# Performance work log

Hardware: AMD Instinct MI355X
Metric: run time of the kernel (lower is better)

## Reference

```python
import jax, jax.numpy as jnp
import numpy as np

N_NODES = 50000
N_EDGES = 800000
D_IN = 128
D_GAT = 128
D_LIN = 512
D_OUT = 4
N_CONVS = 3


def setup_inputs() -> dict:
    key = jax.random.key(0)
    ks = jax.random.split(key, 16)
    s = 1.0 / np.sqrt(D_GAT)
    inp = {
        "x": jax.random.normal(ks[0], (N_NODES, D_IN), dtype=jnp.float32),
        "edge_index": jax.random.randint(ks[1], (2, N_EDGES), 0, N_NODES, dtype=jnp.int64),
        # 3 GATConv layers (input_dim == hidden_gat_dim so params stack)
        "conv_W": jax.random.normal(ks[2], (N_CONVS, D_GAT, D_GAT), dtype=jnp.float32) * s,
        "conv_a_src": jax.random.normal(ks[3], (N_CONVS, D_GAT), dtype=jnp.float32) * s,
        "conv_a_dst": jax.random.normal(ks[4], (N_CONVS, D_GAT), dtype=jnp.float32) * s,
        "conv_b": jnp.zeros((N_CONVS, D_GAT), dtype=jnp.float32),
        # MLP head: 128->512, 512->512, 512->512, 512->4
        "lin_W0": jax.random.normal(ks[5], (D_GAT, D_LIN), dtype=jnp.float32) / np.sqrt(D_GAT),
        "lin_b0": jnp.zeros((D_LIN,), dtype=jnp.float32),
        "lin_W1": jax.random.normal(ks[6], (D_LIN, D_LIN), dtype=jnp.float32) / np.sqrt(D_LIN),
        "lin_b1": jnp.zeros((D_LIN,), dtype=jnp.float32),
        "lin_W2": jax.random.normal(ks[7], (D_LIN, D_LIN), dtype=jnp.float32) / np.sqrt(D_LIN),
        "lin_b2": jnp.zeros((D_LIN,), dtype=jnp.float32),
        "lin_Wout": jax.random.normal(ks[8], (D_LIN, D_OUT), dtype=jnp.float32) / np.sqrt(D_LIN),
        "lin_bout": jnp.zeros((D_OUT,), dtype=jnp.float32),
    }
    return inp


def _gat_layer(x, src, dst, W, a_src, a_dst, b, n):
    """PyG-style single-head GATConv with self loops already in (src, dst)."""
    h = x @ W                                    # [N, F]
    e = (h @ a_src)[src] + (h @ a_dst)[dst]      # per-edge raw score [E]
    e = jax.nn.leaky_relu(e, 0.2)
    # segment softmax over destination node neighborhoods
    m = jax.ops.segment_max(e, dst, num_segments=n)
    ex = jnp.exp(e - m[dst])
    denom = jax.ops.segment_sum(ex, dst, num_segments=n)
    alpha = ex / denom[dst]                      # [E]
    out = jax.ops.segment_sum(alpha[:, None] * h[src], dst, num_segments=n)
    return out + b


def reference(x, edge_index, conv_W, conv_a_src, conv_a_dst, conv_b,
              lin_W0, lin_b0, lin_W1, lin_b1, lin_W2, lin_b2, lin_Wout, lin_bout):
    n = x.shape[0]
    loops = jnp.arange(n, dtype=edge_index.dtype)
    src = jnp.concatenate([edge_index[0], loops])  # add self loops (PyG default)
    dst = jnp.concatenate([edge_index[1], loops])
    for i in range(N_CONVS):
        x = _gat_layer(x, src, dst, conv_W[i], conv_a_src[i], conv_a_dst[i], conv_b[i], n)
        x = jax.nn.leaky_relu(x, 0.2)
    for W, b in ((lin_W0, lin_b0), (lin_W1, lin_b1), (lin_W2, lin_b2)):
        x = jax.nn.relu(x @ W + b)  # F.relu(x, 0.2): 0.2 is truthy inplace flag -> plain relu
    return x @ lin_Wout + lin_bout
```

## Files before the change

kernel.cpp:

```cpp
#include <hip/hip_runtime.h>
#include <hip/hip_bf16.h>

#define NN 50000
#define NE 800000
#define NET (NE + NN)
#define SCAN_NB ((NN + 255) / 256)

static inline int imin(int a, int b) { return a < b ? a : b; }

typedef _Float16 half8 __attribute__((ext_vector_type(8)));
typedef _Float16 half2v __attribute__((ext_vector_type(2)));
typedef float f32x4 __attribute__((ext_vector_type(4)));

__global__ void k_count(const int* __restrict__ edst, int* __restrict__ counts) {
    int e = blockIdx.x * blockDim.x + threadIdx.x;
    if (e >= NET) return;
    int d = (e < NE) ? edst[e] : (e - NE);
    atomicAdd(&counts[d], 1);
}

__global__ __launch_bounds__(256) void k_scan1(const int* __restrict__ counts,
                                               int* __restrict__ part) {
    __shared__ int s[256];
    int t = threadIdx.x, i = blockIdx.x * 256 + t;
    s[t] = (i < NN) ? counts[i] : 0;
    __syncthreads();
    for (int off = 128; off > 0; off >>= 1) {
        if (t < off) s[t] += s[t + off];
        __syncthreads();
    }
    if (t == 0) part[blockIdx.x] = s[0];
}

__global__ __launch_bounds__(256) void k_scan2(int* __restrict__ part, int* __restrict__ offs) {
    __shared__ int s[256];
    int t = threadIdx.x;
    int v = (t < SCAN_NB) ? part[t] : 0;
    s[t] = v;
    __syncthreads();
    for (int off = 1; off < 256; off <<= 1) {
        int a = (t >= off) ? s[t - off] : 0;
        __syncthreads();
        s[t] += a;
        __syncthreads();
    }
    if (t < SCAN_NB) part[t] = s[t] - v;
    if (t == 255) offs[NN] = s[255];
}

__global__ __launch_bounds__(256) void k_scan3(const int* __restrict__ counts,
                                               const int* __restrict__ part,
                                               int* __restrict__ offs, int* __restrict__ cursor) {
    __shared__ int s[256];
    int t = threadIdx.x, i = blockIdx.x * 256 + t;
    int v = (i < NN) ? counts[i] : 0;
    s[t] = v;
    __syncthreads();
    for (int off = 1; off < 256; off <<= 1) {
        int a = (t >= off) ? s[t - off] : 0;
        __syncthreads();
        s[t] += a;
        __syncthreads();
    }
    if (i < NN) {
        int e = part[blockIdx.x] + s[t] - v;
        offs[i] = e;
        cursor[i] = e;
    }
}

__global__ void k_scatter(const int* __restrict__ esrc, const int* __restrict__ edst,
                          int* __restrict__ cursor, int* __restrict__ csr_src) {
    int e = blockIdx.x * blockDim.x + threadIdx.x;
    if (e >= NET) return;
    int s, d;
    if (e < NE) { s = esrc[e]; d = edst[e]; } else { s = e - NE; d = s; }
    int pos = atomicAdd(&cursor[d], 1);
    csr_src[pos] = s;
}

__global__ void k_split(const float* __restrict__ in, _Float16* __restrict__ hi,
                        _Float16* __restrict__ lo, int n) {
    int i = blockIdx.x * blockDim.x + threadIdx.x;
    int st = gridDim.x * blockDim.x;
    for (; i < n; i += st) {
        float v = in[i];
        _Float16 h = (_Float16)v;
        hi[i] = h;
        lo[i] = (_Float16)(v - (float)h);
    }
}

__global__ __launch_bounds__(256) void k_prepw(const float* __restrict__ W,
                                               _Float16* __restrict__ Th,
                                               _Float16* __restrict__ Tl, int K, int N) {
    __shared__ float tile[32][33];
    int tx = threadIdx.x & 31, ty = threadIdx.x >> 5;
    int n0 = blockIdx.x * 32, k0 = blockIdx.y * 32;
    #pragma unroll
    for (int r = ty; r < 32; r += 8)
        tile[r][tx] = W[(size_t)(k0 + r) * N + n0 + tx];
    __syncthreads();
    #pragma unroll
    for (int r = ty; r < 32; r += 8) {
        int n = n0 + r, k = k0 + tx;
        float v = tile[tx][r];
        _Float16 h = (_Float16)v;
        Th[(size_t)n * K + k] = h;
        Tl[(size_t)n * K + k] = (_Float16)(v - (float)h);
    }
}

__global__ void k_aggregate(const _Float16* __restrict__ h, const float* __restrict__ s_src,
                            const float* __restrict__ s_dst, const int* __restrict__ offs,
                            const int* __restrict__ csr_src, const float* __restrict__ bias,
                            _Float16* __restrict__ xh, _Float16* __restrict__ xl) {
    int node = blockIdx.x * 4 + (threadIdx.x >> 6);
    int lane = threadIdx.x & 63;
    if (node >= NN) return;
    int p = offs[node], pe = offs[node + 1];
    float sd = s_dst[node];
    float den = 0.f, acc0 = 0.f, acc1 = 0.f;
    for (; p + 4 <= pe; p += 4) {
        int s0 = csr_src[p + 0], s1 = csr_src[p + 1];
        int s2 = csr_src[p + 2], s3 = csr_src[p + 3];
        float e0 = s_src[s0] + sd, e1 = s_src[s1] + sd;
        float e2 = s_src[s2] + sd, e3 = s_src[s3] + sd;
        half2v a0 = *((const half2v*)(h + (size_t)s0 * 128) + lane);
        half2v a1 = *((const half2v*)(h + (size_t)s1 * 128) + lane);
        half2v a2 = *((const half2v*)(h + (size_t)s2 * 128) + lane);
        half2v a3 = *((const half2v*)(h + (size_t)s3 * 128) + lane);
        e0 = (e0 > 0.f) ? e0 : 0.2f * e0;  float w0 = __expf(e0);
        e1 = (e1 > 0.f) ? e1 : 0.2f * e1;  float w1 = __expf(e1);
        e2 = (e2 > 0.f) ? e2 : 0.2f * e2;  float w2 = __expf(e2);
        e3 = (e3 > 0.f) ? e3 : 0.2f * e3;  float w3 = __expf(e3);
        den += (w0 + w1) + (w2 + w3);
        acc0 += w0 * (float)a0[0] + w1 * (float)a1[0] + w2 * (float)a2[0] + w3 * (float)a3[0];
        acc1 += w0 * (float)a0[1] + w1 * (float)a1[1] + w2 * (float)a2[1] + w3 * (float)a3[1];
    }
    for (; p < pe; ++p) {
        int src = csr_src[p];
        float e = s_src[src] + sd;
        e = (e > 0.f) ? e : 0.2f * e;
        float wgt = __expf(e);
        den += wgt;
        half2v av = *((const half2v*)(h + (size_t)src * 128) + lane);
        acc0 += wgt * (float)av[0];
        acc1 += wgt * (float)av[1];
    }
    float inv = 1.f / den;
    float2 bv = *((const float2*)bias + lane);
    float v0 = acc0 * inv + bv.x;
    float v1 = acc1 * inv + bv.y;
    v0 = (v0 > 0.f) ? v0 : 0.2f * v0;
    v1 = (v1 > 0.f) ? v1 : 0.2f * v1;
    _Float16 h0 = (_Float16)v0, h1 = (_Float16)v1;
    size_t base = (size_t)node * 128 + 2 * lane;
    *(half2v*)(xh + base) = (half2v){h0, h1};
    *(half2v*)(xl + base) = (half2v){(_Float16)(v0 - (float)h0), (_Float16)(v1 - (float)h1)};
}

__device__ __forceinline__ void gload_lds16(const void* g, void* l) {
    __builtin_amdgcn_global_load_lds(
        (const __attribute__((address_space(1))) void*)g,
        (__attribute__((address_space(3))) void*)l, 16, 0, 0);
}

__device__ __forceinline__ void phase_stagger(int bid) {
    int ph = (int)(((unsigned)bid * 2654435761u) >> 29);
    for (int i = 0; i < ph; ++i) __builtin_amdgcn_s_sleep(8);
}

__global__ __launch_bounds__(512) void k_mgemm(
    const _Float16* __restrict__ Ahi, const _Float16* __restrict__ Alo,
    const _Float16* __restrict__ Bhi, const _Float16* __restrict__ Blo,
    const float* __restrict__ bias, float* __restrict__ Cf,
    _Float16* __restrict__ Chi, _Float16* __restrict__ Clo,
    int M, int N, int K, int relu, int split, int nx, int ntiles)
{
    __shared__ _Float16 sm[4][2][128][32];

    int bid = blockIdx.x;
    int per = (ntiles + 7) >> 3;
    int g = (bid & 7) * per + (bid >> 3);
    if (g >= ntiles) return;
    int col0 = (g % nx) * 128;
    int row0 = (g / nx) * 128;

    phase_stagger(bid);

    int t = threadIdx.x;
    int w = t >> 6, lane = t & 63;
    int wm = (w & 3) * 32, wn = (w >> 2) * 64;
    int fr = lane & 15;
    int fq = lane >> 4, fq8 = fq * 8;

    int srow = t >> 2;
    int scol = (t & 3) << 3;
    int lrow = w << 4;

    f32x4 acc[2][4];
    #pragma unroll
    for (int i = 0; i < 2; i++)
        #pragma unroll
        for (int j = 0; j < 4; j++) acc[i][j] = (f32x4){0.f, 0.f, 0.f, 0.f};

    for (int k0 = 0; k0 < K; k0 += 64) {
        if (k0) __syncthreads();
        {
            int ga = row0 + srow; if (ga > M - 1) ga = M - 1;
            int gb = col0 + srow;
            #pragma unroll
            for (int kk = 0; kk < 2; ++kk) {
                int kc = k0 + kk * 32 + scol;
                gload_lds16(Ahi + (size_t)ga * K + kc, &sm[0][kk][lrow][0]);
                gload_lds16(Alo + (size_t)ga * K + kc, &sm[1][kk][lrow][0]);
                gload_lds16(Bhi + (size_t)gb * K + kc, &sm[2][kk][lrow][0]);
                gload_lds16(Blo + (size_t)gb * K + kc, &sm[3][kk][lrow][0]);
            }
        }
        __syncthreads();

        #pragma unroll
        for (int kk = 0; kk < 2; ++kk) {
            half8 bh[4], bl[4];
            #pragma unroll
            for (int ni = 0; ni < 4; ++ni) {
                bh[ni] = *(half8*)&sm[2][kk][wn + ni * 16 + fr][fq8];
                bl[ni] = *(half8*)&sm[3][kk][wn + ni * 16 + fr][fq8];
            }
            #pragma unroll
            for (int mi = 0; mi < 2; ++mi) {
                half8 ah = *(half8*)&sm[0][kk][wm + mi * 16 + fr][fq8];
                half8 al = *(half8*)&sm[1][kk][wm + mi * 16 + fr][fq8];
                #pragma unroll
                for (int ni = 0; ni < 4; ++ni) {
                    acc[mi][ni] = __builtin_amdgcn_mfma_f32_16x16x32_f16(ah, bh[ni], acc[mi][ni], 0, 0, 0);
                    acc[mi][ni] = __builtin_amdgcn_mfma_f32_16x16x32_f16(ah, bl[ni], acc[mi][ni], 0, 0, 0);
                    acc[mi][ni] = __builtin_amdgcn_mfma_f32_16x16x32_f16(al, bh[ni], acc[mi][ni], 0, 0, 0);
                }
            }
        }
    }

    float bv[4];
    #pragma unroll
    for (int ni = 0; ni < 4; ++ni)
        bv[ni] = bias ? bias[col0 + wn + ni * 16 + fr] : 0.f;

    if (split) {
        _Float16* sc = &sm[0][0][0][0];
        #pragma unroll
        for (int pass = 0; pass < 2; ++pass) {
            __syncthreads();
            #pragma unroll
            for (int mi = 0; mi < 2; ++mi) {
                #pragma unroll
                for (int ni = 0; ni < 4; ++ni) {
                    #pragma unroll
                    for (int r = 0; r < 4; ++r) {
                        int row = wm + mi * 16 + fq * 4 + r;
                        int col = wn + ni * 16 + fr;
                        float v = acc[mi][ni][r] + bv[ni];
                        if (relu) v = (v > 0.f) ? v : 0.f;
                        _Float16 hh = (_Float16)v;
                        sc[row * 128 + col] = pass ? (_Float16)(v - (float)hh) : hh;
                    }
                }
            }
            __syncthreads();
            _Float16* dst = pass ? Clo : Chi;
            #pragma unroll
            for (int pp = 0; pp < 4; ++pp) {
                int idx = t + pp * 512;
                int row = idx >> 4, seg = idx & 15;
                int gr = row0 + row;
                if (gr < M)
                    *(half8*)(dst + (size_t)gr * N + col0 + seg * 8) =
                        *(half8*)&sc[row * 128 + seg * 8];
            }
        }
    } else {
        #pragma unroll
        for (int ni = 0; ni < 4; ++ni) {
            #pragma unroll
            for (int mi = 0; mi < 2; ++mi) {
                #pragma unroll
                for (int r = 0; r < 4; ++r) {
                    int gr = row0 + wm + mi * 16 + fq * 4 + r;
                    if (gr >= M) continue;
                    float v = acc[mi][ni][r] + bv[ni];
                    if (relu) v = (v > 0.f) ? v : 0.f;
                    Cf[(size_t)gr * N + col0 + wn + ni * 16 + fr] = v;
                }
            }
        }
    }
}

__global__ __launch_bounds__(512) void k_mgemm_gat(
    const _Float16* __restrict__ Ahi, const _Float16* __restrict__ Alo,
    const _Float16* __restrict__ Bhi, const _Float16* __restrict__ Blo,
    const float* __restrict__ a_src, const float* __restrict__ a_dst,
    _Float16* __restrict__ hbuf, float* __restrict__ s_src, float* __restrict__ s_dst,
    int M, int ntiles)
{
    __shared__ _Float16 sm[4][2][128][32];
    __shared__ float sps[2][128], spd[2][128];

    const int K = 128;
    int bid = blockIdx.x;
    int per = (ntiles + 7) >> 3;
    int g = (bid & 7) * per + (bid >> 3);
    if (g >= ntiles) return;
    int row0 = g * 128;

    int t = threadIdx.x;
    int w = t >> 6, lane = t & 63;
    int wm = (w & 3) * 32, wn = (w >> 2) * 64;
    int fr = lane & 15;
    int fq = lane >> 4, fq8 = fq * 8;
    int wnIdx = w >> 2;

    int srow = t >> 2;
    int scol = (t & 3) << 3;
    int lrow = w << 4;

    f32x4 acc[2][4];
    #pragma unroll
    for (int i = 0; i < 2; i++)
        #pragma unroll
        for (int j = 0; j < 4; j++) acc[i][j] = (f32x4){0.f, 0.f, 0.f, 0.f};

    for (int k0 = 0; k0 < K; k0 += 64) {
        if (k0) __syncthreads();
        {
            int ga = row0 + srow; if (ga > M - 1) ga = M - 1;
            int gb = srow;
            #pragma unroll
            for (int kk = 0; kk < 2; ++kk) {
                int kc = k0 + kk * 32 + scol;
                gload_lds16(Ahi + (size_t)ga * K + kc, &sm[0][kk][lrow][0]);
                gload_lds16(Alo + (size_t)ga * K + kc, &sm[1][kk][lrow][0]);
                gload_lds16(Bhi + (size_t)gb * K + kc, &sm[2][kk][lrow][0]);
                gload_lds16(Blo + (size_t)gb * K + kc, &sm[3][kk][lrow][0]);
            }
        }
        __syncthreads();

        #pragma unroll
        for (int kk = 0; kk < 2; ++kk) {
            half8 bh[4], bl[4];
            #pragma unroll
            for (int ni = 0; ni < 4; ++ni) {
                bh[ni] = *(half8*)&sm[2][kk][wn + ni * 16 + fr][fq8];
                bl[ni] = *(half8*)&sm[3][kk][wn + ni * 16 + fr][fq8];
            }
            #pragma unroll
            for (int mi = 0; mi < 2; ++mi) {
                half8 ah = *(half8*)&sm[0][kk][wm + mi * 16 + fr][fq8];
                half8 al = *(half8*)&sm[1][kk][wm + mi * 16 + fr][fq8];
                #pragma unroll
                for (int ni = 0; ni < 4; ++ni) {
                    acc[mi][ni] = __builtin_amdgcn_mfma_f32_16x16x32_f16(ah, bh[ni], acc[mi][ni], 0, 0, 0);
                    acc[mi][ni] = __builtin_amdgcn_mfma_f32_16x16x32_f16(ah, bl[ni], acc[mi][ni], 0, 0, 0);
                    acc[mi][ni] = __builtin_amdgcn_mfma_f32_16x16x32_f16(al, bh[ni], acc[mi][ni], 0, 0, 0);
                }
            }
        }
    }

    float asv[4], adv[4];
    #pragma unroll
    for (int ni = 0; ni < 4; ++ni) {
        int gc = wn + ni * 16 + fr;
        asv[ni] = a_src[gc];
        adv[ni] = a_dst[gc];
    }
    __syncthreads();
    _Float16* sc = &sm[0][0][0][0];
    #pragma unroll
    for (int mi = 0; mi < 2; ++mi) {
        #pragma unroll
        for (int r = 0; r < 4; ++r) {
            int row = wm + mi * 16 + fq * 4 + r;
            float vps = 0.f, vpd = 0.f;
            #pragma unroll
            for (int ni = 0; ni < 4; ++ni) {
                float v = acc[mi][ni][r];
                vps += v * asv[ni];
                vpd += v * adv[ni];
                sc[row * 128 + wn + ni * 16 + fr] = (_Float16)v;
            }
            #pragma unroll
            for (int off = 1; off < 16; off <<= 1) {
                vps += __shfl_xor(vps, off);
                vpd += __shfl_xor(vpd, off);
            }
            if (fr == 0) { sps[wnIdx][row] = vps; spd[wnIdx][row] = vpd; }
        }
    }
    __syncthreads();
    if (t < 128) {
        int gr = row0 + t;
        if (gr < M) {
            s_src[gr] = sps[0][t] + sps[1][t];
            s_dst[gr] = spd[0][t] + spd[1][t];
        }
    }
    #pragma unroll
    for (int pp = 0; pp < 4; ++pp) {
        int idx = t + pp * 512;
        int row = idx >> 4, seg = idx & 15;
        int gr = row0 + row;
        if (gr < M)
            *(half8*)(hbuf + (size_t)gr * 128 + seg * 8) = *(half8*)&sc[row * 128 + seg * 8];
    }
}

__global__ __launch_bounds__(512) void k_mgemm_head(
    const _Float16* __restrict__ Ahi, const _Float16* __restrict__ Alo,
    const _Float16* __restrict__ Bhi, const _Float16* __restrict__ Blo,
    const float* __restrict__ bias, const float* __restrict__ Wo,
    float* __restrict__ partial,
    int M, int K, int nx, int ntiles)
{
    __shared__ _Float16 sm[4][2][128][32];
    __shared__ float4 sacc[2][128];

    int bid = blockIdx.x;
    int per = (ntiles + 7) >> 3;
    int g = (bid & 7) * per + (bid >> 3);
    if (g >= ntiles) return;
    int ct = g % nx;
    int col0 = ct * 128;
    int row0 = (g / nx) * 128;

    phase_stagger(bid);

    int t = threadIdx.x;
    int w = t >> 6, lane = t & 63;
    int wm = (w & 3) * 32, wn = (w >> 2) * 64;
    int fr = lane & 15;
    int fq = lane >> 4, fq8 = fq * 8;

    int srow = t >> 2;
    int scol = (t & 3) << 3;
    int lrow = w << 4;

    f32x4 acc[2][4];
    #pragma unroll
    for (int i = 0; i < 2; i++)
        #pragma unroll
        for (int j = 0; j < 4; j++) acc[i][j] = (f32x4){0.f, 0.f, 0.f, 0.f};

    for (int k0 = 0; k0 < K; k0 += 64) {
        if (k0) __syncthreads();
        {
            int ga = row0 + srow; if (ga > M - 1) ga = M - 1;
            int gb = col0 + srow;
            #pragma unroll
            for (int kk = 0; kk < 2; ++kk) {
                int kc = k0 + kk * 32 + scol;
                gload_lds16(Ahi + (size_t)ga * K + kc, &sm[0][kk][lrow][0]);
                gload_lds16(Alo + (size_t)ga * K + kc, &sm[1][kk][lrow][0]);
                gload_lds16(Bhi + (size_t)gb * K + kc, &sm[2][kk][lrow][0]);
                gload_lds16(Blo + (size_t)gb * K + kc, &sm[3][kk][lrow][0]);
            }
        }
        __syncthreads();

        #pragma unroll
        for (int kk = 0; kk < 2; ++kk) {
            half8 bh[4], bl[4];
            #pragma unroll
            for (int ni = 0; ni < 4; ++ni) {
                bh[ni] = *(half8*)&sm[2][kk][wn + ni * 16 + fr][fq8];
                bl[ni] = *(half8*)&sm[3][kk][wn + ni * 16 + fr][fq8];
            }
            #pragma unroll
            for (int mi = 0; mi < 2; ++mi) {
                half8 ah = *(half8*)&sm[0][kk][wm + mi * 16 + fr][fq8];
                half8 al = *(half8*)&sm[1][kk][wm + mi * 16 + fr][fq8];
                #pragma unroll
                for (int ni = 0; ni < 4; ++ni) {
                    acc[mi][ni] = __builtin_amdgcn_mfma_f32_16x16x32_f16(ah, bh[ni], acc[mi][ni], 0, 0, 0);
                    acc[mi][ni] = __builtin_amdgcn_mfma_f32_16x16x32_f16(ah, bl[ni], acc[mi][ni], 0, 0, 0);
                    acc[mi][ni] = __builtin_amdgcn_mfma_f32_16x16x32_f16(al, bh[ni], acc[mi][ni], 0, 0, 0);
                }
            }
        }
    }

    float bv[4];
    float4 wv[4];
    #pragma unroll
    for (int ni = 0; ni < 4; ++ni) {
        int gc = col0 + wn + ni * 16 + fr;
        bv[ni] = bias[gc];
        wv[ni] = *(const float4*)(Wo + (size_t)gc * 4);
    }
    #pragma unroll
    for (int mi = 0; mi < 2; ++mi) {
        #pragma unroll
        for (int r = 0; r < 4; ++r) {
            int row = wm + mi * 16 + fq * 4 + r;
            float o0 = 0.f, o1 = 0.f, o2 = 0.f, o3 = 0.f;
            #pragma unroll
            for (int ni = 0; ni < 4; ++ni) {
                float v = acc[mi][ni][r] + bv[ni];
                v = (v > 0.f) ? v : 0.f;
                o0 += v * wv[ni].x; o1 += v * wv[ni].y;
                o2 += v * wv[ni].z; o3 += v * wv[ni].w;
            }
            #pragma unroll
            for (int off = 1; off < 16; off <<= 1) {
                o0 += __shfl_xor(o0, off); o1 += __shfl_xor(o1, off);
                o2 += __shfl_xor(o2, off); o3 += __shfl_xor(o3, off);
            }
            if (fr == 0) sacc[w >> 2][row] = (float4){o0, o1, o2, o3};
        }
    }
    __syncthreads();
    if (t < 128) {
        int gr = row0 + t;
        if (gr < M) {
            float4 s0 = sacc[0][t], s1 = sacc[1][t];
            float4 o = (float4){s0.x + s1.x, s0.y + s1.y, s0.z + s1.z, s0.w + s1.w};
            *(float4*)(partial + ((size_t)ct * M + gr) * 4) = o;
        }
    }
}

__global__ __launch_bounds__(256) void k_headred(const float* __restrict__ partial,
                                                 const float* __restrict__ bo,
                                                 float* __restrict__ out, int M) {
    int r = blockIdx.x * 256 + threadIdx.x;
    if (r >= M) return;
    float4 a = *(const float4*)(partial + ((size_t)0 * M + r) * 4);
    float4 b = *(const float4*)(partial + ((size_t)1 * M + r) * 4);
    float4 c = *(const float4*)(partial + ((size_t)2 * M + r) * 4);
    float4 d = *(const float4*)(partial + ((size_t)3 * M + r) * 4);
    float4 o;
    o.x = a.x + b.x + c.x + d.x + bo[0];
    o.y = a.y + b.y + c.y + d.y + bo[1];
    o.z = a.z + b.z + c.z + d.z + bo[2];
    o.w = a.w + b.w + c.w + d.w + bo[3];
    *(float4*)(out + (size_t)r * 4) = o;
}

extern "C" void kernel_launch(void* const* d_in, const int* in_sizes, int n_in,
                              void* d_out, int out_size, void* d_ws, size_t ws_size,
                              hipStream_t stream) {
    const float* x    = (const float*)d_in[0];
    const int*   eidx = (const int*)d_in[1];
    const float* cW   = (const float*)d_in[2];
    const float* caS  = (const float*)d_in[3];
    const float* caD  = (const float*)d_in[4];
    const float* cB   = (const float*)d_in[5];
    const float* W0   = (const float*)d_in[6];
    const float* b0   = (const float*)d_in[7];
    const float* W1   = (const float*)d_in[8];
    const float* b1   = (const float*)d_in[9];
    const float* W2   = (const float*)d_in[10];
    const float* b2   = (const float*)d_in[11];
    const float* Wo   = (const float*)d_in[12];
    const float* bo   = (const float*)d_in[13];
    (void)in_sizes; (void)n_in; (void)out_size;

    const int* esrc = eidx;
    const int* edst = eidx + NE;
    float* out = (float*)d_out;

    char* w = (char*)d_ws;
    auto alloc = [&](size_t bytes) -> char* {
        char* p = w;
        w += (bytes + 255) & ~(size_t)255;
        return p;
    };
    _Float16* x0h  = (_Float16*)alloc((size_t)NN * 128 * 2);
    _Float16* x0l  = (_Float16*)alloc((size_t)NN * 128 * 2);
    _Float16* xh   = (_Float16*)alloc((size_t)NN * 128 * 2);
    _Float16* xl   = (_Float16*)alloc((size_t)NN * 128 * 2);
    _Float16* hbuf = (_Float16*)alloc((size_t)NN * 128 * 2);
    float* ssrc    = (float*)alloc((size_t)NN * 4);
    float* sdst    = (float*)alloc((size_t)NN * 4);
    int*   counts  = (int*)  alloc((size_t)NN * 4);
    int*   offs    = (int*)  alloc((size_t)(NN + 1) * 4);
    int*   cursor  = (int*)  alloc((size_t)NN * 4);
    int*   csr     = (int*)  alloc((size_t)NET * 4);
    int*   part    = (int*)  alloc((size_t)SCAN_NB * 4);
    _Float16* cwh  = (_Float16*)alloc(3 * 128 * 128 * 2);
    _Float16* cwl  = (_Float16*)alloc(3 * 128 * 128 * 2);
    _Float16* w0h  = (_Float16*)alloc(512 * 128 * 2);
    _Float16* w0l  = (_Float16*)alloc(512 * 128 * 2);
    _Float16* w1h  = (_Float16*)alloc(512 * 512 * 2);
    _Float16* w1l  = (_Float16*)alloc(512 * 512 * 2);
    _Float16* w2h  = (_Float16*)alloc(512 * 512 * 2);
    _Float16* w2l  = (_Float16*)alloc(512 * 512 * 2);
    float* hpart   = (float*)alloc((size_t)4 * NN * 4 * 4);

    size_t used = (size_t)(w - (char*)d_ws);
    size_t rem = (ws_size > used) ? (ws_size - used) : 0;
    int chunk = (int)(rem / (4 * 512 * sizeof(_Float16)));
    if (chunk > NN) chunk = NN;
    if (chunk > 128) chunk &= ~127;
    if (chunk < 1) chunk = 1;
    _Float16* Y0h = (_Float16*)alloc((size_t)chunk * 512 * 2);
    _Float16* Y0l = (_Float16*)alloc((size_t)chunk * 512 * 2);
    _Float16* Y1h = (_Float16*)alloc((size_t)chunk * 512 * 2);
    _Float16* Y1l = (_Float16*)alloc((size_t)chunk * 512 * 2);

    auto gemm = [&](const _Float16* Ah, const _Float16* Al,
                    const _Float16* Bh, const _Float16* Bl,
                    const float* bias, float* Cf, _Float16* Ch, _Float16* Cl,
                    int M, int N, int K, int relu, int split) {
        int nx = N / 128;
        int ntiles = nx * ((M + 127) / 128);
        int nb = ((ntiles + 7) / 8) * 8;
        k_mgemm<<<nb, 512, 0, stream>>>(Ah, Al, Bh, Bl, bias, Cf, Ch, Cl,
                                        M, N, K, relu, split, nx, ntiles);
    };

    k_split<<<2048, 256, 0, stream>>>(x, x0h, x0l, NN * 128);
    for (int L = 0; L < 3; ++L)
        k_prepw<<<dim3(128 / 32, 128 / 32), 256, 0, stream>>>(
            cW + (size_t)L * 128 * 128, cwh + (size_t)L * 128 * 128, cwl + (size_t)L * 128 * 128, 128, 128);
    k_prepw<<<dim3(512 / 32, 128 / 32), 256, 0, stream>>>(W0, w0h, w0l, 128, 512);
    k_prepw<<<dim3(512 / 32, 512 / 32), 256, 0, stream>>>(W1, w1h, w1l, 512, 512);
    k_prepw<<<dim3(512 / 32, 512 / 32), 256, 0, stream>>>(W2, w2h, w2l, 512, 512);

    hipMemsetAsync(counts, 0, (size_t)NN * 4, stream);
    int eblocks = (NET + 255) / 256;
    k_count <<<eblocks, 256, 0, stream>>>(edst, counts);
    k_scan1 <<<SCAN_NB, 256, 0, stream>>>(counts, part);
    k_scan2 <<<1, 256, 0, stream>>>(part, offs);
    k_scan3 <<<SCAN_NB, 256, 0, stream>>>(counts, part, offs, cursor);
    k_scatter<<<eblocks, 256, 0, stream>>>(esrc, edst, cursor, csr);

    int gat_tiles = (NN + 127) / 128;
    int gat_nb = ((gat_tiles + 7) / 8) * 8;
    for (int L = 0; L < 3; ++L) {
        const _Float16* Ah = (L == 0) ? x0h : xh;
        const _Float16* Al = (L == 0) ? x0l : xl;
        k_mgemm_gat<<<gat_nb, 512, 0, stream>>>(
            Ah, Al, cwh + (size_t)L * 128 * 128, cwl + (size_t)L * 128 * 128,
            caS + L * 128, caD + L * 128, hbuf, ssrc, sdst, NN, gat_tiles);
        k_aggregate<<<NN / 4, 256, 0, stream>>>(hbuf, ssrc, sdst, offs, csr, cB + L * 128, xh, xl);
    }

    for (int m0 = 0; m0 < NN; m0 += chunk) {
        int cm = imin(chunk, NN - m0);
        gemm(xh + (size_t)m0 * 128, xl + (size_t)m0 * 128, w0h, w0l, b0,
             nullptr, Y0h, Y0l, cm, 512, 128, 1, 1);
        gemm(Y0h, Y0l, w1h, w1l, b1, nullptr, Y1h, Y1l, cm, 512, 512, 1, 1);
        int nx = 4;
        int ntiles = nx * ((cm + 127) / 128);
        int nb = ((ntiles + 7) / 8) * 8;
        k_mgemm_head<<<nb, 512, 0, stream>>>(Y1h, Y1l, w2h, w2l, b2, Wo,
                                             hpart, cm, 512, nx, ntiles);
        k_headred<<<(cm + 255) / 256, 256, 0, stream>>>(hpart, bo, out + (size_t)m0 * 4, cm);
    }
}
```

Measured before the change: 639.3 us.

## Double-buffer LDS tiles in split-fp16 MFMA GEMM kernels to overlap loads with compute

Both MLP GEMM kernels switch from a single 64-wide K stage (load, sync, compute, sync) to a ping-pong pair of 32-wide K LDS buffers. The next tile is prefetched via global_load_lds while MFMAs run on the current one, with an explicit vmcnt wait and barrier per step. This aims to hide global-load latency behind compute, at the cost of twice as many barriers per K and shallower per-step work.

New measurement: 641.6 us. About the same (+0.3%).

```diff
diff --git a/kernel.cpp b/kernel.cpp
--- a/kernel.cpp
+++ b/kernel.cpp
@@ -178,7 +178,7 @@
     _Float16* __restrict__ Chi, _Float16* __restrict__ Clo,
     int M, int N, int K, int relu, int split, int nx, int ntiles)
 {
-    __shared__ _Float16 sm[4][2][128][32];
+    __shared__ _Float16 sm[2][4][128][32];
 
     int bid = blockIdx.x;
     int per = (ntiles + 7) >> 3;
@@ -199,48 +199,55 @@
     int scol = (t & 3) << 3;
     int lrow = w << 4;
 
+    int ga = row0 + srow; if (ga > M - 1) ga = M - 1;
+    int gb = col0 + srow;
+
     f32x4 acc[2][4];
     #pragma unroll
     for (int i = 0; i < 2; i++)
         #pragma unroll
         for (int j = 0; j < 4; j++) acc[i][j] = (f32x4){0.f, 0.f, 0.f, 0.f};
 
-    for (int k0 = 0; k0 < K; k0 += 64) {
-        if (k0) __syncthreads();
-        {
-            int ga = row0 + srow; if (ga > M - 1) ga = M - 1;
-            int gb = col0 + srow;
-            #pragma unroll
-            for (int kk = 0; kk < 2; ++kk) {
-                int kc = k0 + kk * 32 + scol;
-                gload_lds16(Ahi + (size_t)ga * K + kc, &sm[0][kk][lrow][0]);
-                gload_lds16(Alo + (size_t)ga * K + kc, &sm[1][kk][lrow][0]);
-                gload_lds16(Bhi + (size_t)gb * K + kc, &sm[2][kk][lrow][0]);
-                gload_lds16(Blo + (size_t)gb * K + kc, &sm[3][kk][lrow][0]);
-            }
-        }
-        __syncthreads();
-
-        #pragma unroll
-        for (int kk = 0; kk < 2; ++kk) {
-            half8 bh[4], bl[4];
+    auto STAGE = [&](int buf, int k0) {
+        int kc = k0 + scol;
+        gload_lds16(Ahi + (size_t)ga * K + kc, &sm[buf][0][lrow][0]);
+        gload_lds16(Alo + (size_t)ga * K + kc, &sm[buf][1][lrow][0]);
+        gload_lds16(Bhi + (size_t)gb * K + kc, &sm[buf][2][lrow][0]);
+        gload_lds16(Blo + (size_t)gb * K + kc, &sm[buf][3][lrow][0]);
+    };
+
+    STAGE(0, 0);
+    asm volatile("s_waitcnt vmcnt(0)" ::: "memory");
+    __builtin_amdgcn_s_barrier();
+    asm volatile("" ::: "memory");
+
+    int NT = K >> 5;
+    for (int tt = 0; tt < NT; ++tt) {
+        int cur = tt & 1;
+        if (tt + 1 < NT) STAGE(cur ^ 1, (tt + 1) << 5);
+        asm volatile("" ::: "memory");
+
+        half8 bh[4], bl[4];
+        #pragma unroll
+        for (int ni = 0; ni < 4; ++ni) {
+            bh[ni] = *(half8*)&sm[cur][2][wn + ni * 16 + fr][fq8];
+            bl[ni] = *(half8*)&sm[cur][3][wn + ni * 16 + fr][fq8];
+        }
+        #pragma unroll
+        for (int mi = 0; mi < 2; ++mi) {
+            half8 ah = *(half8*)&sm[cur][0][wm + mi * 16 + fr][fq8];
+            half8 al = *(half8*)&sm[cur][1][wm + mi * 16 + fr][fq8];
             #pragma unroll
             for (int ni = 0; ni < 4; ++ni) {
-                bh[ni] = *(half8*)&sm[2][kk][wn + ni * 16 + fr][fq8];
-                bl[ni] = *(half8*)&sm[3][kk][wn + ni * 16 + fr][fq8];
-            }
-            #pragma unroll
-            for (int mi = 0; mi < 2; ++mi) {
-                half8 ah = *(half8*)&sm[0][kk][wm + mi * 16 + fr][fq8];
-                half8 al = *(half8*)&sm[1][kk][wm + mi * 16 + fr][fq8];
-                #pragma unroll
-                for (int ni = 0; ni < 4; ++ni) {
-                    acc[mi][ni] = __builtin_amdgcn_mfma_f32_16x16x32_f16(ah, bh[ni], acc[mi][ni], 0, 0, 0);
-                    acc[mi][ni] = __builtin_amdgcn_mfma_f32_16x16x32_f16(ah, bl[ni], acc[mi][ni], 0, 0, 0);
-                    acc[mi][ni] = __builtin_amdgcn_mfma_f32_16x16x32_f16(al, bh[ni], acc[mi][ni], 0, 0, 0);
-                }
-            }
-        }
+                acc[mi][ni] = __builtin_amdgcn_mfma_f32_16x16x32_f16(ah, bh[ni], acc[mi][ni], 0, 0, 0);
+                acc[mi][ni] = __builtin_amdgcn_mfma_f32_16x16x32_f16(ah, bl[ni], acc[mi][ni], 0, 0, 0);
+                acc[mi][ni] = __builtin_amdgcn_mfma_f32_16x16x32_f16(al, bh[ni], acc[mi][ni], 0, 0, 0);
+            }
+        }
+
+        asm volatile("s_waitcnt vmcnt(0)" ::: "memory");
+        __builtin_amdgcn_s_barrier();
+        asm volatile("" ::: "memory");
     }
 
     float bv[4];
@@ -425,7 +432,7 @@
     float* __restrict__ partial,
     int M, int K, int nx, int ntiles)
 {
-    __shared__ _Float16 sm[4][2][128][32];
+    __shared__ _Float16 sm[2][4][128][32];
     __shared__ float4 sacc[2][128];
 
     int bid = blockIdx.x;
@@ -448,48 +455,55 @@
     int scol = (t & 3) << 3;
     int lrow = w << 4;
 
+    int ga = row0 + srow; if (ga > M - 1) ga = M - 1;
+    int gb = col0 + srow;
+
     f32x4 acc[2][4];
     #pragma unroll
     for (int i = 0; i < 2; i++)
         #pragma unroll
         for (int j = 0; j < 4; j++) acc[i][j] = (f32x4){0.f, 0.f, 0.f, 0.f};
 
-    for (int k0 = 0; k0 < K; k0 += 64) {
-        if (k0) __syncthreads();
-        {
-            int ga = row0 + srow; if (ga > M - 1) ga = M - 1;
-            int gb = col0 + srow;
-            #pragma unroll
-            for (int kk = 0; kk < 2; ++kk) {
-                int kc = k0 + kk * 32 + scol;
-                gload_lds16(Ahi + (size_t)ga * K + kc, &sm[0][kk][lrow][0]);
-                gload_lds16(Alo + (size_t)ga * K + kc, &sm[1][kk][lrow][0]);
-                gload_lds16(Bhi + (size_t)gb * K + kc, &sm[2][kk][lrow][0]);
-                gload_lds16(Blo + (size_t)gb * K + kc, &sm[3][kk][lrow][0]);
-            }
-        }
-        __syncthreads();
-
-        #pragma unroll
-        for (int kk = 0; kk < 2; ++kk) {
-            half8 bh[4], bl[4];
+    auto STAGE = [&](int buf, int k0) {
+        int kc = k0 + scol;
+        gload_lds16(Ahi + (size_t)ga * K + kc, &sm[buf][0][lrow][0]);
+        gload_lds16(Alo + (size_t)ga * K + kc, &sm[buf][1][lrow][0]);
+        gload_lds16(Bhi + (size_t)gb * K + kc, &sm[buf][2][lrow][0]);
+        gload_lds16(Blo + (size_t)gb * K + kc, &sm[buf][3][lrow][0]);
+    };
+
+    STAGE(0, 0);
+    asm volatile("s_waitcnt vmcnt(0)" ::: "memory");
+    __builtin_amdgcn_s_barrier();
+    asm volatile("" ::: "memory");
+
+    int NT = K >> 5;
+    for (int tt = 0; tt < NT; ++tt) {
+        int cur = tt & 1;
+        if (tt + 1 < NT) STAGE(cur ^ 1, (tt + 1) << 5);
+        asm volatile("" ::: "memory");
+
+        half8 bh[4], bl[4];
+        #pragma unroll
+        for (int ni = 0; ni < 4; ++ni) {
+            bh[ni] = *(half8*)&sm[cur][2][wn + ni * 16 + fr][fq8];
+            bl[ni] = *(half8*)&sm[cur][3][wn + ni * 16 + fr][fq8];
+        }
+        #pragma unroll
+        for (int mi = 0; mi < 2; ++mi) {
+            half8 ah = *(half8*)&sm[cur][0][wm + mi * 16 + fr][fq8];
+            half8 al = *(half8*)&sm[cur][1][wm + mi * 16 + fr][fq8];
             #pragma unroll
             for (int ni = 0; ni < 4; ++ni) {
-                bh[ni] = *(half8*)&sm[2][kk][wn + ni * 16 + fr][fq8];
-                bl[ni] = *(half8*)&sm[3][kk][wn + ni * 16 + fr][fq8];
-            }
-            #pragma unroll
-            for (int mi = 0; mi < 2; ++mi) {
-                half8 ah = *(half8*)&sm[0][kk][wm + mi * 16 + fr][fq8];
-                half8 al = *(half8*)&sm[1][kk][wm + mi * 16 + fr][fq8];
-                #pragma unroll
-                for (int ni = 0; ni < 4; ++ni) {
-                    acc[mi][ni] = __builtin_amdgcn_mfma_f32_16x16x32_f16(ah, bh[ni], acc[mi][ni], 0, 0, 0);
-                    acc[mi][ni] = __builtin_amdgcn_mfma_f32_16x16x32_f16(ah, bl[ni], acc[mi][ni], 0, 0, 0);
-                    acc[mi][ni] = __builtin_amdgcn_mfma_f32_16x16x32_f16(al, bh[ni], acc[mi][ni], 0, 0, 0);
-                }
-            }
-        }
+                acc[mi][ni] = __builtin_amdgcn_mfma_f32_16x16x32_f16(ah, bh[ni], acc[mi][ni], 0, 0, 0);
+                acc[mi][ni] = __builtin_amdgcn_mfma_f32_16x16x32_f16(ah, bl[ni], acc[mi][ni], 0, 0, 0);
+                acc[mi][ni] = __builtin_amdgcn_mfma_f32_16x16x32_f16(al, bh[ni], acc[mi][ni], 0, 0, 0);
+            }
+        }
+
+        asm volatile("s_waitcnt vmcnt(0)" ::: "memory");
+        __builtin_amdgcn_s_barrier();
+        asm volatile("" ::: "memory");
     }
 
     float bv[4];
```
